# Optimization experiments

Measured on AMD Instinct MI355X. Metric: run time of the kernel, lower is better.

The kernel has to match this reference:

```python
import jax, jax.numpy as jnp
import numpy as np

EMBED = 1024
HEADS = 16
HEAD_DIM = EMBED // HEADS


def setup_inputs() -> dict:
    key = jax.random.key(0)
    ks = jax.random.split(key, 9)
    s = 1.0 / np.sqrt(EMBED)
    inp = {
        "x": jax.random.normal(ks[0], (2, 2048, EMBED), dtype=jnp.float32),
        "wq": jax.random.uniform(ks[1], (EMBED, EMBED), jnp.float32, -s, s),
        "bq": jax.random.uniform(ks[2], (EMBED,), jnp.float32, -s, s),
        "wk": jax.random.uniform(ks[3], (EMBED, EMBED), jnp.float32, -s, s),
        "bk": jax.random.uniform(ks[4], (EMBED,), jnp.float32, -s, s),
        "wv": jax.random.uniform(ks[5], (EMBED, EMBED), jnp.float32, -s, s),
        "bv": jax.random.uniform(ks[6], (EMBED,), jnp.float32, -s, s),
        "wo": jax.random.uniform(ks[7], (EMBED, EMBED), jnp.float32, -s, s),
        "bo": jax.random.uniform(ks[8], (EMBED,), jnp.float32, -s, s),
    }
    return inp


def reference(x, wq, bq, wk, bk, wv, bv, wo, bo):
    B, S, E = x.shape
    H, D = HEADS, HEAD_DIM
    # projections (torch Linear: y = x @ W.T + b; here weights stored as [E, E] applied as x @ W.T)
    q = (x @ wq.T + bq).reshape(B, S, H, D).transpose(0, 2, 1, 3)  # [B,H,S,D]
    k = (x @ wk.T + bk).reshape(B, S, H, D).transpose(0, 2, 1, 3)
    v = (x @ wv.T + bv).reshape(B, S, H, D).transpose(0, 2, 1, 3)
    scores = jnp.einsum("bhqd,bhkd->bhqk", q, k) / jnp.sqrt(jnp.asarray(D, x.dtype))
    attn = jax.nn.softmax(scores, axis=-1)  # dropout is identity in eval / p=0
    ctx = jnp.einsum("bhqk,bhkd->bhqd", attn, v)
    ctx = ctx.transpose(0, 2, 1, 3).reshape(B, S, E)
    return ctx @ wo.T + bo
```

## Files before the change

kernel.cpp:

```cpp
#include <hip/hip_runtime.h>
#include <hip/hip_bf16.h>

#define EMBED 1024
#define HEADS 16
#define HDIM  64
#define BATCH 2
#define SEQ   2048
#define MTOT  (BATCH*SEQ)

typedef __attribute__((ext_vector_type(8))) short bf16x8;
typedef __attribute__((ext_vector_type(4))) short bf16x4;
typedef __attribute__((ext_vector_type(4))) float f32x4;
typedef __attribute__((ext_vector_type(8))) unsigned short u16x8;
typedef __attribute__((ext_vector_type(2))) unsigned u32x2;
typedef __attribute__((ext_vector_type(4))) unsigned u32x4;

__device__ __forceinline__ unsigned pack2(float lo, float hi) {
    __hip_bfloat162 h = __float22bfloat162_rn(make_float2(lo, hi));
    unsigned u;
    __builtin_memcpy(&u, &h, sizeof(u));
    return u;
}
__device__ __forceinline__ unsigned short f2bf(float f) {
    __hip_bfloat16 h = __float2bfloat16(f);
    unsigned short u;
    __builtin_memcpy(&u, &h, sizeof(u));
    return u;
}
__device__ __forceinline__ u16x8 cvt8(float4 a, float4 b) {
    u32x4 r;
    r[0] = pack2(a.x, a.y);
    r[1] = pack2(a.z, a.w);
    r[2] = pack2(b.x, b.y);
    r[3] = pack2(b.z, b.w);
    return __builtin_bit_cast(u16x8, r);
}

__device__ __forceinline__ f32x4 mfma16(bf16x4 a, bf16x4 b, f32x4 c) {
#if __has_builtin(__builtin_amdgcn_mfma_f32_16x16x16bf16_1k)
    return __builtin_amdgcn_mfma_f32_16x16x16bf16_1k(a, b, c, 0, 0, 0);
#else
    f32x4 d;
    asm volatile("v_mfma_f32_16x16x16_bf16 %0, %1, %2, %3"
                 : "=v"(d) : "v"(a), "v"(b), "v"(c));
    return d;
#endif
}

__global__ __launch_bounds__(256, 2) void qkv_proj(
    const float* __restrict__ x,
    const float* __restrict__ wq, const float* __restrict__ bq,
    const float* __restrict__ wk, const float* __restrict__ bk,
    const float* __restrict__ wv, const float* __restrict__ bv,
    unsigned short* __restrict__ qo,
    unsigned short* __restrict__ ko,
    unsigned short* __restrict__ vto)
{
    const int which = blockIdx.z;
    const float* __restrict__ w    = (which == 0) ? wq : (which == 1) ? wk : wv;
    const float* __restrict__ bias = (which == 0) ? bq : (which == 1) ? bk : bv;
    const float kscale = (which == 1) ? 0.18033688f : 1.0f;

    const int m0 = blockIdx.x * 128;
    const int n0 = blockIdx.y * 128;

    __shared__ unsigned short a_lds[128][40];
    __shared__ unsigned short b_lds[128][40];

    const int tid  = threadIdx.x;
    const int lane = tid & 63;
    const int wid  = tid >> 6;
    const int wr   = wid >> 1, wc = wid & 1;
    const int lq   = lane & 15;
    const int lg   = lane >> 4;

    f32x4 acc[4][4] = {};

    const int srow = tid >> 2;
    const int scol = (tid & 3) * 8;

    for (int k0 = 0; k0 < EMBED; k0 += 32) {
        #pragma unroll
        for (int p = 0; p < 2; ++p) {
            const int r = srow + p * 64;
            const float4* sa = (const float4*)(x + (size_t)(m0 + r) * EMBED + k0 + scol);
            *(u16x8*)&a_lds[r][scol] = cvt8(sa[0], sa[1]);
            const float4* sb = (const float4*)(w + (size_t)(n0 + r) * EMBED + k0 + scol);
            *(u16x8*)&b_lds[r][scol] = cvt8(sb[0], sb[1]);
        }
        __syncthreads();
        bf16x8 af[4], bfr[4];
        #pragma unroll
        for (int i = 0; i < 4; ++i)
            af[i] = *(const bf16x8*)&a_lds[wr*64 + i*16 + lq][lg*8];
        #pragma unroll
        for (int j = 0; j < 4; ++j)
            bfr[j] = *(const bf16x8*)&b_lds[wc*64 + j*16 + lq][lg*8];
        #pragma unroll
        for (int i = 0; i < 4; ++i)
            #pragma unroll
            for (int j = 0; j < 4; ++j)
                acc[i][j] = __builtin_amdgcn_mfma_f32_16x16x32_bf16(af[i], bfr[j], acc[i][j], 0, 0, 0);
        __syncthreads();
    }

    #pragma unroll
    for (int j = 0; j < 4; ++j) {
        const int nn = n0 + wc*64 + j*16 + lq;
        const float bsv = bias[nn];
        const int h = nn >> 6, d = nn & (HDIM-1);
        #pragma unroll
        for (int i = 0; i < 4; ++i) {
            const int mmb = m0 + wr*64 + i*16 + lg*4;
            const int b = mmb >> 11;
            const int s = mmb & (SEQ-1);
            const size_t bh = (size_t)(b*HEADS + h);
            if (which == 2) {
                u32x2 ov;
                ov[0] = pack2(acc[i][j][0] + bsv, acc[i][j][1] + bsv);
                ov[1] = pack2(acc[i][j][2] + bsv, acc[i][j][3] + bsv);
                *(u32x2*)&vto[(bh*HDIM + d)*SEQ + s] = ov;
            } else {
                unsigned short* o = (which == 0) ? qo : ko;
                #pragma unroll
                for (int r = 0; r < 4; ++r)
                    o[(bh*SEQ + (s + r))*HDIM + d] = f2bf((acc[i][j][r] + bsv) * kscale);
            }
        }
    }
}

__global__ __launch_bounds__(256, 4) void attn(
    const unsigned short* __restrict__ q,
    const unsigned short* __restrict__ k,
    const unsigned short* __restrict__ vt,
    unsigned short* __restrict__ ctx)
{
    __shared__ __align__(16) unsigned char sm[2 * 16384];

    const int bid   = blockIdx.x;
    const int xcd   = bid & 7;
    const int local = bid >> 3;
    const int bh    = xcd * 4 + (local >> 5);
    const int q0    = (local & 31) * 64;
    const int b     = bh >> 4;
    const int h     = bh & (HEADS - 1);
    const int tid   = threadIdx.x;
    const int wv    = tid >> 6;
    const int lane  = tid & 63;
    const int lq = lane & 15, lg = lane >> 4;

    const unsigned short* qb = q  + (size_t)bh * SEQ * HDIM;
    const unsigned short* kb = k  + (size_t)bh * SEQ * HDIM;
    const unsigned short* vb = vt + (size_t)bh * HDIM * SEQ;

    const int swz    = (lq & 7) << 4;
    const int kread0 = lq*128 + ((lg*16)      ^ swz);
    const int kread1 = lq*128 + ((lg*16 + 64) ^ swz);

    const int vrd0 = lq*128 + ((lg*32)      ^ swz);
    const int vrd1 = lq*128 + ((lg*32 + 16) ^ swz);

    const int wrow = tid >> 3;
    const int c8   = tid & 7;
    const int wswz = (wrow & 7) << 4;
    const int woff = wrow*128 + ((c8 * 16) ^ wswz);
    const int vin0 = (c8 & 1)*64 + (c8 >> 1)*8;
    const int woffV0 = wrow*128 + (vin0        ^ wswz);
    const int woffV1 = wrow*128 + ((vin0 + 32) ^ wswz);

    const int scol = c8 * 8;
    const unsigned short* kp = kb + (size_t)wrow * HDIM + scol;
    const unsigned short* vp = vb + (size_t)wrow * SEQ + scol;

    bf16x8 qf[2];
    #pragma unroll
    for (int hh = 0; hh < 2; ++hh)
        qf[hh] = *(const bf16x8*)(qb + (size_t)(q0 + wv*16 + lq) * HDIM + hh*32 + lg*8);

    f32x4 o[4] = {};
    float lr = 0.f;

    u16x8 kr0, kr1, vr0, vr1;

#define LOADT() do {                                                           \
    kr0 = *(const u16x8*)(kp);                                                 \
    kr1 = *(const u16x8*)(kp + 32*HDIM);                                       \
    vr0 = *(const u16x8*)(vp);                                                 \
    vr1 = *(const u16x8*)(vp + 32*SEQ);                                        \
} while (0)

#define WRITET(BF) do {                                                        \
    unsigned char* smb = sm + (BF)*16384;                                      \
    *(u16x8*)(smb +        woff) = kr0;                                        \
    *(u16x8*)(smb + 4096 + woff) = kr1;                                        \
    u32x4 t0 = __builtin_bit_cast(u32x4, vr0);                                 \
    u32x4 t1 = __builtin_bit_cast(u32x4, vr1);                                 \
    u32x2 hlf;                                                                 \
    hlf[0] = t0[0]; hlf[1] = t0[1];                                            \
    *(u32x2*)(smb +  8192 + woffV0) = hlf;                                     \
    hlf[0] = t0[2]; hlf[1] = t0[3];                                            \
    *(u32x2*)(smb +  8192 + woffV1) = hlf;                                     \
    hlf[0] = t1[0]; hlf[1] = t1[1];                                            \
    *(u32x2*)(smb + 12288 + woffV0) = hlf;                                     \
    hlf[0] = t1[2]; hlf[1] = t1[3];                                            \
    *(u32x2*)(smb + 12288 + woffV1) = hlf;                                     \
} while (0)

#define COMPUTE(BF) do {                                                       \
    const unsigned char* smb = sm + (BF)*16384;                                \
    f32x4 s_[4];                                                               \
    _Pragma("unroll")                                                          \
    for (int sub = 0; sub < 4; ++sub) {                                        \
        bf16x8 k0 = *(const bf16x8*)(smb + sub*2048 + kread0);                 \
        bf16x8 k1 = *(const bf16x8*)(smb + sub*2048 + kread1);                 \
        f32x4 z = {};                                                          \
        z = __builtin_amdgcn_mfma_f32_16x16x32_bf16(k0, qf[0], z, 0, 0, 0);    \
        z = __builtin_amdgcn_mfma_f32_16x16x32_bf16(k1, qf[1], z, 0, 0, 0);    \
        s_[sub] = z;                                                           \
    }                                                                          \
    bf16x4 pf[4];                                                              \
    float psum = 0.f;                                                          \
    _Pragma("unroll")                                                          \
    for (int sub = 0; sub < 4; ++sub) {                                        \
        f32x4 pv;                                                              \
        _Pragma("unroll")                                                      \
        for (int r = 0; r < 4; ++r) pv[r] = exp2f(s_[sub][r]);                 \
        psum += (pv[0] + pv[1]) + (pv[2] + pv[3]);                             \
        u32x2 pk;                                                              \
        pk[0] = pack2(pv[0], pv[1]);                                           \
        pk[1] = pack2(pv[2], pv[3]);                                           \
        pf[sub] = __builtin_bit_cast(bf16x4, pk);                              \
    }                                                                          \
    lr += psum;                                                                \
    _Pragma("unroll")                                                          \
    for (int i = 0; i < 4; ++i) {                                              \
        bf16x8 v01 = *(const bf16x8*)(smb + 8192 + i*2048 + vrd0);             \
        bf16x8 v23 = *(const bf16x8*)(smb + 8192 + i*2048 + vrd1);             \
        u32x4 a01 = __builtin_bit_cast(u32x4, v01);                            \
        u32x4 a23 = __builtin_bit_cast(u32x4, v23);                            \
        u32x2 hw;                                                              \
        hw[0] = a01[0]; hw[1] = a01[1];                                        \
        o[i] = mfma16(__builtin_bit_cast(bf16x4, hw), pf[0], o[i]);            \
        hw[0] = a01[2]; hw[1] = a01[3];                                        \
        o[i] = mfma16(__builtin_bit_cast(bf16x4, hw), pf[1], o[i]);            \
        hw[0] = a23[0]; hw[1] = a23[1];                                        \
        o[i] = mfma16(__builtin_bit_cast(bf16x4, hw), pf[2], o[i]);            \
        hw[0] = a23[2]; hw[1] = a23[3];                                        \
        o[i] = mfma16(__builtin_bit_cast(bf16x4, hw), pf[3], o[i]);            \
    }                                                                          \
} while (0)

    LOADT();
    WRITET(0);
    __syncthreads();
    kp += 64 * HDIM;
    vp += 64;

    for (int t2 = 0; t2 < 16; ++t2) {
        {
            const int t = 2 * t2;
            if (t < 31) LOADT();
            COMPUTE(0);
            if (t < 31) {
                WRITET(1);
                __syncthreads();
                kp += 64 * HDIM;
                vp += 64;
            }
        }
        {
            const int t = 2 * t2 + 1;
            if (t < 31) LOADT();
            COMPUTE(1);
            if (t < 31) {
                WRITET(0);
                __syncthreads();
                kp += 64 * HDIM;
                vp += 64;
            }
        }
    }

#undef LOADT
#undef WRITET
#undef COMPUTE

    float lm = lr + __shfl_xor(lr, 16);
    lm += __shfl_xor(lm, 32);
    const float inv = 1.0f / lm;
    unsigned short* cb = ctx + ((size_t)(b*SEQ + q0 + wv*16 + lq)) * EMBED + h*HDIM;
    #pragma unroll
    for (int i = 0; i < 4; ++i) {
        u32x2 ov;
        ov[0] = pack2(o[i][0] * inv, o[i][1] * inv);
        ov[1] = pack2(o[i][2] * inv, o[i][3] * inv);
        *(u32x2*)(cb + i*16 + lg*4) = ov;
    }
}

__global__ __launch_bounds__(256, 2) void out_proj(
    const unsigned short* __restrict__ ctx,
    const float* __restrict__ wo, const float* __restrict__ bo,
    float* __restrict__ out)
{
    const int m0 = blockIdx.x * 128;
    const int n0 = blockIdx.y * 128;

    __shared__ unsigned short a_lds[128][40];
    __shared__ unsigned short b_lds[128][40];

    const int tid  = threadIdx.x;
    const int lane = tid & 63;
    const int wid  = tid >> 6;
    const int wr   = wid >> 1, wc = wid & 1;
    const int lq   = lane & 15;
    const int lg   = lane >> 4;

    f32x4 acc[4][4] = {};

    const int srow = tid >> 2;
    const int scol = (tid & 3) * 8;

    for (int k0 = 0; k0 < EMBED; k0 += 32) {
        #pragma unroll
        for (int p = 0; p < 2; ++p) {
            const int r = srow + p * 64;
            *(u16x8*)&a_lds[r][scol] =
                *(const u16x8*)(ctx + (size_t)(m0 + r) * EMBED + k0 + scol);
            const float4* sb = (const float4*)(wo + (size_t)(n0 + r) * EMBED + k0 + scol);
            *(u16x8*)&b_lds[r][scol] = cvt8(sb[0], sb[1]);
        }
        __syncthreads();
        bf16x8 af[4], bfr[4];
        #pragma unroll
        for (int i = 0; i < 4; ++i)
            af[i] = *(const bf16x8*)&a_lds[wr*64 + i*16 + lq][lg*8];
        #pragma unroll
        for (int j = 0; j < 4; ++j)
            bfr[j] = *(const bf16x8*)&b_lds[wc*64 + j*16 + lq][lg*8];
        #pragma unroll
        for (int i = 0; i < 4; ++i)
            #pragma unroll
            for (int j = 0; j < 4; ++j)
                acc[i][j] = __builtin_amdgcn_mfma_f32_16x16x32_bf16(af[i], bfr[j], acc[i][j], 0, 0, 0);
        __syncthreads();
    }

    #pragma unroll
    for (int j = 0; j < 4; ++j) {
        const int nn = n0 + wc*64 + j*16 + lq;
        const float bsv = bo[nn];
        #pragma unroll
        for (int i = 0; i < 4; ++i) {
            const int mm = m0 + wr*64 + i*16 + lg*4;
            #pragma unroll
            for (int r = 0; r < 4; ++r)
                out[(size_t)(mm + r) * EMBED + nn] = acc[i][j][r] + bsv;
        }
    }
}

extern "C" void kernel_launch(void* const* d_in, const int* in_sizes, int n_in,
                              void* d_out, int out_size, void* d_ws, size_t ws_size,
                              hipStream_t stream) {
    const float* x  = (const float*)d_in[0];
    const float* wq = (const float*)d_in[1];
    const float* bq = (const float*)d_in[2];
    const float* wk = (const float*)d_in[3];
    const float* bk = (const float*)d_in[4];
    const float* wv = (const float*)d_in[5];
    const float* bv = (const float*)d_in[6];
    const float* wo = (const float*)d_in[7];
    const float* bo = (const float*)d_in[8];
    float* out = (float*)d_out;

    const size_t NELEM = (size_t)MTOT * EMBED;
    unsigned short* q_ws   = (unsigned short*)d_ws;
    unsigned short* k_ws   = q_ws  + NELEM;
    unsigned short* vt_ws  = k_ws  + NELEM;
    unsigned short* ctx_ws = vt_ws + NELEM;

    qkv_proj<<<dim3(MTOT/128, EMBED/128, 3), 256, 0, stream>>>(
        x, wq, bq, wk, bk, wv, bv, q_ws, k_ws, vt_ws);
    attn<<<dim3(SEQ/64 * BATCH*HEADS), 256, 0, stream>>>(q_ws, k_ws, vt_ws, ctx_ws);
    out_proj<<<dim3(MTOT/128, EMBED/128), 256, 0, stream>>>(ctx_ws, wo, bo, out);
}
```

Measured before the change: 150.4 us.

## Pre-convert inputs and weights to bf16 in a separate kernel before GEMMs

Adds a preconvert kernel that converts x and all four weight matrices from fp32 to bf16 once per call. The projection GEMMs then load bf16 tiles directly instead of re-reading fp32 and converting inside the k-loop. This halves global/L2 traffic for repeatedly-read tiles and removes conversion ALU work from the inner loop, at the cost of an extra launch and a full read/write pass. xb reuses the ctx workspace, and the weights need extra workspace.

New measurement: 145.5 us. -3.3%, faster.

```diff
diff --git a/kernel.cpp b/kernel.cpp
--- a/kernel.cpp
+++ b/kernel.cpp
@@ -26,14 +26,6 @@
     unsigned short u;
     __builtin_memcpy(&u, &h, sizeof(u));
     return u;
-}
-__device__ __forceinline__ u16x8 cvt8(float4 a, float4 b) {
-    u32x4 r;
-    r[0] = pack2(a.x, a.y);
-    r[1] = pack2(a.z, a.w);
-    r[2] = pack2(b.x, b.y);
-    r[3] = pack2(b.z, b.w);
-    return __builtin_bit_cast(u16x8, r);
 }
 
 __device__ __forceinline__ f32x4 mfma16(bf16x4 a, bf16x4 b, f32x4 c) {
@@ -47,17 +39,48 @@
 #endif
 }
 
+__global__ __launch_bounds__(256) void preconvert(
+    const float* __restrict__ x,
+    const float* __restrict__ wq, const float* __restrict__ wk,
+    const float* __restrict__ wv, const float* __restrict__ wo,
+    unsigned short* __restrict__ xb,
+    unsigned short* __restrict__ wqb, unsigned short* __restrict__ wkb,
+    unsigned short* __restrict__ wvb, unsigned short* __restrict__ wob)
+{
+    const int NX = (MTOT * EMBED) / 4;
+    const int NW = (EMBED * EMBED) / 4;
+    int idx = blockIdx.x * 256 + threadIdx.x;
+    const float* src;
+    unsigned short* dst;
+    int off;
+    if (idx < NX) {
+        src = x; dst = xb; off = idx;
+    } else {
+        int r = idx - NX;
+        int w = r / NW;
+        off = r - w * NW;
+        src = (w == 0) ? wq : (w == 1) ? wk : (w == 2) ? wv : wo;
+        dst = (w == 0) ? wqb : (w == 1) ? wkb : (w == 2) ? wvb : wob;
+    }
+    float4 v = ((const float4*)src)[off];
+    u32x2 o;
+    o[0] = pack2(v.x, v.y);
+    o[1] = pack2(v.z, v.w);
+    *(u32x2*)(dst + (size_t)off * 4) = o;
+}
+
 __global__ __launch_bounds__(256, 2) void qkv_proj(
-    const float* __restrict__ x,
-    const float* __restrict__ wq, const float* __restrict__ bq,
-    const float* __restrict__ wk, const float* __restrict__ bk,
-    const float* __restrict__ wv, const float* __restrict__ bv,
+    const unsigned short* __restrict__ xb,
+    const unsigned short* __restrict__ wqb, const float* __restrict__ bq,
+    const unsigned short* __restrict__ wkb, const float* __restrict__ bk,
+    const unsigned short* __restrict__ wvb, const float* __restrict__ bv,
     unsigned short* __restrict__ qo,
     unsigned short* __restrict__ ko,
     unsigned short* __restrict__ vto)
 {
     const int which = blockIdx.z;
-    const float* __restrict__ w    = (which == 0) ? wq : (which == 1) ? wk : wv;
+    const unsigned short* __restrict__ w =
+        (which == 0) ? wqb : (which == 1) ? wkb : wvb;
     const float* __restrict__ bias = (which == 0) ? bq : (which == 1) ? bk : bv;
     const float kscale = (which == 1) ? 0.18033688f : 1.0f;
 
@@ -83,10 +106,10 @@
         #pragma unroll
         for (int p = 0; p < 2; ++p) {
             const int r = srow + p * 64;
-            const float4* sa = (const float4*)(x + (size_t)(m0 + r) * EMBED + k0 + scol);
-            *(u16x8*)&a_lds[r][scol] = cvt8(sa[0], sa[1]);
-            const float4* sb = (const float4*)(w + (size_t)(n0 + r) * EMBED + k0 + scol);
-            *(u16x8*)&b_lds[r][scol] = cvt8(sb[0], sb[1]);
+            *(u16x8*)&a_lds[r][scol] =
+                *(const u16x8*)(xb + (size_t)(m0 + r) * EMBED + k0 + scol);
+            *(u16x8*)&b_lds[r][scol] =
+                *(const u16x8*)(w + (size_t)(n0 + r) * EMBED + k0 + scol);
         }
         __syncthreads();
         bf16x8 af[4], bfr[4];
@@ -301,7 +324,7 @@
 
 __global__ __launch_bounds__(256, 2) void out_proj(
     const unsigned short* __restrict__ ctx,
-    const float* __restrict__ wo, const float* __restrict__ bo,
+    const unsigned short* __restrict__ wob, const float* __restrict__ bo,
     float* __restrict__ out)
 {
     const int m0 = blockIdx.x * 128;
@@ -328,8 +351,8 @@
             const int r = srow + p * 64;
             *(u16x8*)&a_lds[r][scol] =
                 *(const u16x8*)(ctx + (size_t)(m0 + r) * EMBED + k0 + scol);
-            const float4* sb = (const float4*)(wo + (size_t)(n0 + r) * EMBED + k0 + scol);
-            *(u16x8*)&b_lds[r][scol] = cvt8(sb[0], sb[1]);
+            *(u16x8*)&b_lds[r][scol] =
+                *(const u16x8*)(wob + (size_t)(n0 + r) * EMBED + k0 + scol);
         }
         __syncthreads();
         bf16x8 af[4], bfr[4];
@@ -376,13 +399,22 @@
     float* out = (float*)d_out;
 
     const size_t NELEM = (size_t)MTOT * EMBED;
+    const size_t WELEM = (size_t)EMBED * EMBED;
     unsigned short* q_ws   = (unsigned short*)d_ws;
     unsigned short* k_ws   = q_ws  + NELEM;
     unsigned short* vt_ws  = k_ws  + NELEM;
     unsigned short* ctx_ws = vt_ws + NELEM;
-
+    unsigned short* wqb    = ctx_ws + NELEM;
+    unsigned short* wkb    = wqb + WELEM;
+    unsigned short* wvb    = wkb + WELEM;
+    unsigned short* wob    = wvb + WELEM;
+    unsigned short* xb     = ctx_ws;
+
+    const int NCONV = (int)((NELEM + 4 * WELEM) / 4);
+    preconvert<<<dim3(NCONV / 256), 256, 0, stream>>>(
+        x, wq, wk, wv, wo, xb, wqb, wkb, wvb, wob);
     qkv_proj<<<dim3(MTOT/128, EMBED/128, 3), 256, 0, stream>>>(
-        x, wq, bq, wk, bk, wv, bv, q_ws, k_ws, vt_ws);
+        xb, wqb, bq, wkb, bk, wvb, bv, q_ws, k_ws, vt_ws);
     attn<<<dim3(SEQ/64 * BATCH*HEADS), 256, 0, stream>>>(q_ws, k_ws, vt_ws, ctx_ws);
-    out_proj<<<dim3(MTOT/128, EMBED/128), 256, 0, stream>>>(ctx_ws, wo, bo, out);
-}
+    out_proj<<<dim3(MTOT/128, EMBED/128), 256, 0, stream>>>(ctx_ws, wob, bo, out);
+}
```
